# Kernel tuning notes

Hardware: AMD Instinct MI355X
Metric: run time of the kernel (lower is better)

## Reference

```python
import jax, jax.numpy as jnp
import numpy as np

HEADS = 12
DIM_HEAD = 64
SCALE = DIM_HEAD ** -0.5


def _attn(q, k, v):
    # q: [B, I, D], k/v: [B, J, D]
    sim = jnp.einsum('bid,bjd->bij', q, k)
    a = jax.nn.softmax(sim, axis=-1)
    out = jnp.einsum('bij,bjd->bid', a, v)
    return out, a


def setup_inputs() -> dict:
    key = jax.random.key(0)
    k1, k2, k3 = jax.random.split(key, 3)
    B, F, N, DIM = 8, 8, 196, 768
    x = jax.random.normal(k1, (B, 1 + F * N, DIM), dtype=jnp.float32)
    W_qkv = jax.random.normal(k2, (DIM, 3 * HEADS * DIM_HEAD), dtype=jnp.float32) * (DIM ** -0.5)
    W_out = jax.random.normal(k3, (HEADS * DIM_HEAD, DIM), dtype=jnp.float32) * ((HEADS * DIM_HEAD) ** -0.5)
    b_out = jnp.zeros((DIM,), dtype=jnp.float32)
    return {"x": x, "W_qkv": W_qkv, "W_out": W_out, "b_out": b_out, "f": F}


def reference(x, W_qkv, W_out, b_out, f):
    b, n_tot, dim = x.shape
    h, d = HEADS, DIM_HEAD
    qkv = x @ W_qkv                              # [b, n, 3*h*d]
    q, k, v = jnp.split(qkv, 3, axis=-1)
    # 'b n (h d) -> (b h) n d'
    def to_bh(t):
        return t.reshape(b, n_tot, h, d).transpose(0, 2, 1, 3).reshape(b * h, n_tot, d)
    q, k, v = map(to_bh, (q, k, v))
    q = q * SCALE
    cls_q, q_ = q[:, :1], q[:, 1:]
    cls_k, k_ = k[:, :1], k[:, 1:]
    cls_v, v_ = v[:, :1], v[:, 1:]
    # cls token attends over full sequence
    cls_out, cls_attn = _attn(cls_q, k, v)       # [(b h), 1, d], [(b h), 1, n_tot]
    # spatial attention: 'b (f n) d -> (b f) n d'
    bh = b * h
    n = (n_tot - 1) // f
    def to_bf(t):
        return t.reshape(bh, f, n, d).reshape(bh * f, n, d)
    q_, k_, v_ = map(to_bf, (q_, k_, v_))
    r = f  # q_.shape[0] // cls_k.shape[0]
    # repeat 'b () d -> (b r) () d'
    cls_k_r = jnp.repeat(cls_k, r, axis=0)       # [(bh f), 1, d]
    cls_v_r = jnp.repeat(cls_v, r, axis=0)
    k_ = jnp.concatenate((cls_k_r, k_), axis=1)  # [(bh f), 1+n, d]
    v_ = jnp.concatenate((cls_v_r, v_), axis=1)
    out, _ = _attn(q_, k_, v_)                   # [(bh f), n, d]
    # '(b f) n d -> b (f n) d' (with b := bh)
    out = out.reshape(bh, f * n, d)
    out = jnp.concatenate((cls_out, out), axis=1)  # [(b h), n_tot, d]
    # '(b h) n d -> b n (h d)'
    out = out.reshape(b, h, n_tot, d).transpose(0, 2, 1, 3).reshape(b, n_tot, h * d)
    return out @ W_out + b_out, cls_attn
```

## Files before the change

kernel.cpp:

```cpp
#include <hip/hip_runtime.h>

typedef unsigned short u16;
typedef unsigned int u32;
typedef __attribute__((ext_vector_type(8))) short s16x8;
typedef __attribute__((ext_vector_type(4))) float f32x4;
typedef __attribute__((ext_vector_type(4))) u32 u32x4;
typedef __attribute__((ext_vector_type(4))) float fvec4;

#define DEV static __device__ __forceinline__

typedef __attribute__((address_space(1))) unsigned char ga_u8;
typedef __attribute__((address_space(3))) unsigned char la_u8;

DEV u16 f2bf(float f){
  u32 u = __builtin_bit_cast(u32, f);
  u32 r = (u + 0x7FFFu + ((u >> 16) & 1u)) >> 16;
  return (u16)r;
}
DEV float bf2f(u16 v){
  u32 x = ((u32)v) << 16;
  return __builtin_bit_cast(float, x);
}
DEV f32x4 mfma16(s16x8 a, s16x8 b, f32x4 c){
  return __builtin_amdgcn_mfma_f32_16x16x32_bf16(a, b, c, 0, 0, 0);
}
DEV s16x8 ld16B(const u16* p){
  return __builtin_bit_cast(s16x8, *(const u32x4*)p);
}
DEV u32 cvt_pk_bf16(float lo, float hi){
  u32 r;
  asm volatile("v_cvt_pk_bf16_f32 %0, %1, %2" : "=v"(r) : "v"(lo), "v"(hi));
  return r;
}
DEV void gload16(const void* g, void* l){
  __builtin_amdgcn_global_load_lds((const ga_u8*)g, (la_u8*)l, 16, 0, 0);
}
DEV int xcd_chunk(int bid, int nwg){
  int q = nwg >> 3, r = nwg & 7;
  int xcd = bid & 7, lin = bid >> 3;
  return (xcd < r ? xcd*(q+1) : r*(q+1) + (xcd-r)*q) + lin;
}

#define BARRIER() __builtin_amdgcn_s_barrier()
#define LGKM0()   asm volatile("s_waitcnt lgkmcnt(0)" ::: "memory")
#define VMC4()    asm volatile("s_waitcnt vmcnt(4)" ::: "memory")
#define VMC0()    asm volatile("s_waitcnt vmcnt(0)" ::: "memory")


__global__ __launch_bounds__(256) void k_cvt(const float* __restrict__ in, u16* __restrict__ out, int n4){
  int i = blockIdx.x*256 + threadIdx.x;
  int stride = gridDim.x*256;
  for (; i < n4; i += stride){
    fvec4 v = ((const fvec4*)in)[i];
    u16 o0 = f2bf(v[0]), o1 = f2bf(v[1]), o2 = f2bf(v[2]), o3 = f2bf(v[3]);
    u32 lo = (u32)o0 | ((u32)o1 << 16);
    u32 hi = (u32)o2 | ((u32)o3 << 16);
    ((u32*)out)[2*i]   = lo;
    ((u32*)out)[2*i+1] = hi;
  }
}

__global__ __launch_bounds__(256) void k_transpose(const float* __restrict__ W, u16* __restrict__ WT, int K, int N){
  __shared__ float tile[32][33];
  int bn = blockIdx.x * 32;
  int bk = blockIdx.y * 32;
  int tx = threadIdx.x & 31, ty = threadIdx.x >> 5;
  #pragma unroll
  for (int r = ty; r < 32; r += 8)
    tile[r][tx] = W[(size_t)(bk + r)*N + bn + tx];
  __syncthreads();
  #pragma unroll
  for (int r = ty; r < 32; r += 8)
    WT[(size_t)(bn + r)*K + bk + tx] = f2bf(tile[tx][r]);
}

__global__ __launch_bounds__(512, 2) void gemm_qkv(const u16* __restrict__ A, const u16* __restrict__ BT,
                                                   u16* __restrict__ qout, u16* __restrict__ kout, u16* __restrict__ vout){
  __shared__ u16 sA[2][2][128*64];
  __shared__ u16 sB[2][2][128*64];
  const int M = 12552;
  const int NWG = 50*9;
  int logical = xcd_chunk(blockIdx.x, NWG);
  int bxi = logical % 9, byi = logical / 9;
  int bm = byi * 256, bn = bxi * 256;

  int tid = threadIdx.x;
  int w = tid >> 6, l = tid & 63, l15 = l & 15, l4 = l >> 4;
  int wm = w >> 2, wn = w & 3;
  int swz = (l15 & 7) << 3;

  f32x4 acc[8][4];
  #pragma unroll
  for (int a=0;a<8;a++)
    #pragma unroll
    for (int b=0;b<4;b++) acc[a][b] = (f32x4){0.f,0.f,0.f,0.f};

  auto stageA = [&](int dbuf, int h, int kt){
    #pragma unroll
    for (int i=0;i<2;i++){
      int ci = i*512 + tid;
      int cs = ci ^ ((ci>>3)&7);
      int r = cs>>3, cc = (cs&7)*8;
      int gr = bm + h*128 + r; if (gr >= M) gr = M-1;
      gload16(A + (size_t)gr*768 + kt*64 + cc, &sA[dbuf][h][(i*512 + (w<<6))*8]);
    }
  };
  auto stageB = [&](int dbuf, int h, int kt){
    #pragma unroll
    for (int i=0;i<2;i++){
      int ci = i*512 + tid;
      int cs = ci ^ ((ci>>3)&7);
      int r = cs>>3, cc = (cs&7)*8;
      gload16(BT + (size_t)(bn + h*128 + r)*768 + kt*64 + cc, &sB[dbuf][h][(i*512 + (w<<6))*8]);
    }
  };

  s16x8 af[4][2], bf[4][2];
  #define LDA_(d, mi, kk) ld16B(&sA[d][wm][(((mi)*16 + l15)*64 + (kk)*32 + l4*8) ^ swz])
  #define LDB_(d, ni, kk) ld16B(&sB[d][(wn*64 + (ni)*16 + l15)>>7][((((wn*64 + (ni)*16 + l15)&127))*64 + (kk)*32 + l4*8) ^ swz])
  #define QUAD(MH, NH) do{ \
    __builtin_amdgcn_s_setprio(1); \
    _Pragma("unroll") \
    for (int j=0;j<4;j++){ \
      _Pragma("unroll") \
      for (int n=0;n<2;n++){ \
        acc[(MH)*4+j][(NH)*2+n] = mfma16(af[j][0], bf[(NH)*2+n][0], acc[(MH)*4+j][(NH)*2+n]); \
        acc[(MH)*4+j][(NH)*2+n] = mfma16(af[j][1], bf[(NH)*2+n][1], acc[(MH)*4+j][(NH)*2+n]); \
      } } \
    __builtin_amdgcn_s_setprio(0); }while(0)

  stageA(0,0,0); stageA(0,1,0); stageB(0,0,0); stageB(0,1,0);
  stageA(1,0,1); stageA(1,1,1);
  VMC4();
  BARRIER();

  #pragma unroll 1
  for (int it = 0; it < 6; ++it){
    int kt1 = 2*it + 1;
    bool full = (it < 5);
    #pragma unroll
    for (int j=0;j<4;j++){ af[j][0]=LDA_(0,j,0); af[j][1]=LDA_(0,j,1); }
    #pragma unroll
    for (int n=0;n<2;n++){ bf[n][0]=LDB_(0,n,0); bf[n][1]=LDB_(0,n,1); }
    stageB(1, 0, kt1);
    BARRIER(); LGKM0();
    QUAD(0,0);
    BARRIER();
    #pragma unroll
    for (int n=2;n<4;n++){ bf[n][0]=LDB_(0,n,0); bf[n][1]=LDB_(0,n,1); }
    stageB(1, 1, kt1);
    BARRIER(); LGKM0();
    QUAD(0,1);
    BARRIER();
    #pragma unroll
    for (int j=0;j<4;j++){ af[j][0]=LDA_(0,4+j,0); af[j][1]=LDA_(0,4+j,1); }
    if (full) stageA(0, 0, kt1+1);
    BARRIER(); LGKM0();
    QUAD(1,0);
    BARRIER();
    if (full) stageA(0, 1, kt1+1);
    BARRIER();
    QUAD(1,1);
    if (full) { VMC4(); } else { VMC0(); }
    BARRIER();
    #pragma unroll
    for (int j=0;j<4;j++){ af[j][0]=LDA_(1,j,0); af[j][1]=LDA_(1,j,1); }
    #pragma unroll
    for (int n=0;n<2;n++){ bf[n][0]=LDB_(1,n,0); bf[n][1]=LDB_(1,n,1); }
    if (full) stageB(0, 0, kt1+1);
    BARRIER(); LGKM0();
    QUAD(0,0);
    BARRIER();
    #pragma unroll
    for (int n=2;n<4;n++){ bf[n][0]=LDB_(1,n,0); bf[n][1]=LDB_(1,n,1); }
    if (full) stageB(0, 1, kt1+1);
    BARRIER(); LGKM0();
    QUAD(0,1);
    BARRIER();
    #pragma unroll
    for (int j=0;j<4;j++){ af[j][0]=LDA_(1,4+j,0); af[j][1]=LDA_(1,4+j,1); }
    if (full) stageA(1, 0, kt1+2);
    BARRIER(); LGKM0();
    QUAD(1,0);
    BARRIER();
    if (full) stageA(1, 1, kt1+2);
    BARRIER();
    QUAD(1,1);
    if (full) VMC4();
    BARRIER();
  }
  #undef LDA_
  #undef LDB_
  #undef QUAD

  int which = bn / 768;
  int h = ((bn - which*768) >> 6) + wn;
  u16* dst  = (which==0) ? qout : ((which==1) ? kout : vout);
  float scale = (which==0) ? 0.125f : 1.f;
  #pragma unroll
  for (int mi=0; mi<8; mi++){
    #pragma unroll
    for (int r=0; r<4; r++){
      int m = bm + wm*128 + mi*16 + l4*4 + r;
      if (m >= M) continue;
      int b = m / 1569, t = m - b*1569;
      u16* drow = dst + ((size_t)(b*12 + h)*1569 + t)*64 + l15;
      #pragma unroll
      for (int n=0; n<4; n++)
        drow[n*16] = f2bf(acc[mi][n][r] * scale);
    }
  }
}

__global__ __launch_bounds__(256) void cls_sim(const u16* __restrict__ qb, const u16* __restrict__ kb,
                                               float* __restrict__ sim, float* __restrict__ bmax){
  int c = blockIdx.x, g = blockIdx.y;
  int tid = threadIdx.x;
  __shared__ float qv[64];
  __shared__ float red[256];
  if (tid < 64) qv[tid] = bf2f(qb[(size_t)g*1569*64 + tid]);
  __syncthreads();
  int j = c*256 + tid;
  float s = -1e30f;
  if (j < 1569){
    const u16* kr = kb + ((size_t)g*1569 + j)*64;
    float a = 0.f;
    #pragma unroll
    for (int d0 = 0; d0 < 64; d0 += 8){
      u32x4 u = *(const u32x4*)(kr + d0);
      const u16* us = (const u16*)&u;
      #pragma unroll
      for (int i=0;i<8;i++) a += qv[d0+i]*bf2f(us[i]);
    }
    s = a;
    sim[(size_t)g*1569 + j] = s;
  }
  red[tid] = s; __syncthreads();
  for (int st=128; st>0; st>>=1){ if (tid<st) red[tid] = fmaxf(red[tid], red[tid+st]); __syncthreads(); }
  if (tid == 0) bmax[g*8 + c] = red[0];
}

__global__ __launch_bounds__(256) void cls_fin(float* __restrict__ sim, const float* __restrict__ bmax,
                                               float* __restrict__ attn){
  int g = blockIdx.x, tid = threadIdx.x;
  __shared__ float red[256];
  float m = -1e30f;
  #pragma unroll
  for (int c=0;c<7;c++) m = fmaxf(m, bmax[g*8+c]);
  float ls = 0.f;
  for (int j = tid; j < 1569; j += 256){
    float e = expf(sim[(size_t)g*1569+j] - m);
    sim[(size_t)g*1569+j] = e;
    ls += e;
  }
  red[tid] = ls; __syncthreads();
  for (int st=128; st>0; st>>=1){ if (tid<st) red[tid] += red[tid+st]; __syncthreads(); }
  float inv = 1.f/red[0];
  for (int j = tid; j < 1569; j += 256)
    attn[(size_t)g*1569+j] = sim[(size_t)g*1569+j]*inv;
}

__global__ __launch_bounds__(256) void cls_pv(const float* __restrict__ attn, const u16* __restrict__ vb,
                                              float* __restrict__ pvp){
  int c = blockIdx.x, g = blockIdx.y;
  int tid = threadIdx.x;
  int d = tid & 63, kk = tid >> 6;
  __shared__ float red[256];
  float a = 0.f;
  for (int jj = kk; jj < 256; jj += 4){
    int j = c*256 + jj;
    if (j < 1569) a += attn[(size_t)g*1569+j] * bf2f(vb[((size_t)g*1569+j)*64 + d]);
  }
  red[tid] = a; __syncthreads();
  if (tid < 64) pvp[((size_t)g*7 + c)*64 + tid] = red[tid]+red[tid+64]+red[tid+128]+red[tid+192];
}

__global__ __launch_bounds__(64) void cls_pv_red(const float* __restrict__ pvp, u16* __restrict__ ob){
  int g = blockIdx.x, d = threadIdx.x;
  float s = 0.f;
  #pragma unroll
  for (int c=0;c<7;c++) s += pvp[((size_t)g*7+c)*64 + d];
  ob[(size_t)g*1569*64 + d] = f2bf(s);
}

__global__ __launch_bounds__(256) void k_frame(const u16* __restrict__ qb, const u16* __restrict__ kb,
                                               const u16* __restrict__ vb, u16* __restrict__ ob){
  int g = blockIdx.x;
  int bh = g >> 3, fi = g & 7;
  int tid = threadIdx.x;
  int w = tid >> 6, l = tid & 63;
  int l15 = l & 15, l4 = l >> 4;

  __shared__ u16 Ks[208][72];
  __shared__ u16 Vt[64][232];
  __shared__ u16 Ps[4][64][40];

  const u16* qg = qb + ((size_t)bh*1569 + 1 + fi*196)*64;
  const u16* kg = kb + (size_t)bh*1569*64;
  const u16* vg = vb + (size_t)bh*1569*64;

  {
    int jj = tid >> 3, c = (tid & 7)*8;
    #pragma unroll
    for (int base = 0; base < 224; base += 32){
      int j = base + jj;
      u32x4 kv = {0,0,0,0}, vv = {0,0,0,0};
      if (j < 197){
        int t = (j == 0) ? 0 : (1 + fi*196 + j - 1);
        kv = *(const u32x4*)(kg + (size_t)t*64 + c);
        vv = *(const u32x4*)(vg + (size_t)t*64 + c);
      }
      if (j < 208) *(u32x4*)&Ks[j][c] = kv;
      int jl = j & 31;
      int col = (j & ~31) + ((jl & 15)*2 + (jl >> 4));
      const u16* vp = (const u16*)&vv;
      #pragma unroll
      for (int i=0;i<8;i++) Vt[c+i][col] = vp[i];
    }
  }

  s16x8 qf[4][2];
  #pragma unroll
  for (int mt=0; mt<4; mt++){
    int row = w*64 + mt*16 + l15;
    #pragma unroll
    for (int kk=0; kk<2; kk++){
      if (row < 196) qf[mt][kk] = ld16B(qg + (size_t)row*64 + kk*32 + l4*8);
      else { u32x4 z = {0,0,0,0}; qf[mt][kk] = __builtin_bit_cast(s16x8, z); }
    }
  }

  f32x4 acc[4][4];
  float rsum[4][4];
  #pragma unroll
  for (int a=0;a<4;a++)
    #pragma unroll
    for (int b=0;b<4;b++){ acc[a][b] = (f32x4){0.f,0.f,0.f,0.f}; rsum[a][b] = 0.f; }

  __syncthreads();

  for (int ck = 0; ck < 7; ck++){
    int r0 = ck*32 + l15;
    int r1 = r0 + 16; if (r1 > 207) r1 = 207;
    s16x8 kf0[2], kf1[2];
    #pragma unroll
    for (int kk=0; kk<2; kk++){
      kf0[kk] = ld16B(&Ks[r0][kk*32 + l4*8]);
      kf1[kk] = ld16B(&Ks[r1][kk*32 + l4*8]);
    }
    bool ok0 = (ck*32 + l15) < 197;
    bool ok1 = (ck*32 + 16 + l15) < 197;

    #pragma unroll
    for (int mt=0; mt<4; mt++){
      __builtin_amdgcn_s_setprio(1);
      f32x4 s0 = (f32x4){0.f,0.f,0.f,0.f}, s1 = (f32x4){0.f,0.f,0.f,0.f};
      s0 = mfma16(qf[mt][0], kf0[0], s0);
      s0 = mfma16(qf[mt][1], kf0[1], s0);
      s1 = mfma16(qf[mt][0], kf1[0], s1);
      s1 = mfma16(qf[mt][1], kf1[1], s1);
      __builtin_amdgcn_s_setprio(0);
      #pragma unroll
      for (int r=0; r<4; r++){
        float p0 = ok0 ? __expf(s0[r] - 8.f) : 0.f;
        float p1 = ok1 ? __expf(s1[r] - 8.f) : 0.f;
        rsum[mt][r] += p0 + p1;
        int prow = mt*16 + l4*4 + r;
        *(u32*)&Ps[w][prow][2*l15] = cvt_pk_bf16(p0, p1);
      }
    }

    s16x8 vf[4];
    #pragma unroll
    for (int ntd=0; ntd<4; ntd++) vf[ntd] = ld16B(&Vt[ntd*16 + l15][ck*32 + l4*8]);
    #pragma unroll
    for (int mt=0; mt<4; mt++){
      s16x8 pf = ld16B(&Ps[w][mt*16 + l15][l4*8]);
      __builtin_amdgcn_s_setprio(1);
      #pragma unroll
      for (int ntd=0; ntd<4; ntd++)
        acc[mt][ntd] = mfma16(pf, vf[ntd], acc[mt][ntd]);
      __builtin_amdgcn_s_setprio(0);
    }
  }

  u16* og = ob + ((size_t)bh*1569 + 1 + fi*196)*64;
  #pragma unroll
  for (int mt=0; mt<4; mt++){
    #pragma unroll
    for (int r=0; r<4; r++){
      float rs = rsum[mt][r];
      rs += __shfl_xor(rs, 1);
      rs += __shfl_xor(rs, 2);
      rs += __shfl_xor(rs, 4);
      rs += __shfl_xor(rs, 8);
      int row = w*64 + mt*16 + l4*4 + r;
      if (row < 196){
        float inv = 1.f / rs;
        #pragma unroll
        for (int ntd=0; ntd<4; ntd++)
          og[(size_t)row*64 + ntd*16 + l15] = f2bf(acc[mt][ntd][r] * inv);
      }
    }
  }
}

__global__ __launch_bounds__(512, 2) void gemm_out(const u16* __restrict__ AO, const u16* __restrict__ BT,
                                                   const float* __restrict__ bias, float* __restrict__ C){
  __shared__ u16 sA[2][2][128*64];
  __shared__ u16 sB[2][2][128*64];
  const int M = 12552;
  const int NWG = 50*3;
  int logical = xcd_chunk(blockIdx.x, NWG);
  int bxi = logical % 3, byi = logical / 3;
  int bm = byi * 256, bn = bxi * 256;

  int tid = threadIdx.x;
  int w = tid >> 6, l = tid & 63, l15 = l & 15, l4 = l >> 4;
  int wm = w >> 2, wn = w & 3;
  int swz = (l15 & 7) << 3;

  f32x4 acc[8][4];
  #pragma unroll
  for (int a=0;a<8;a++)
    #pragma unroll
    for (int b=0;b<4;b++) acc[a][b] = (f32x4){0.f,0.f,0.f,0.f};

  auto stageA = [&](int dbuf, int h, int kt){
    #pragma unroll
    for (int i=0;i<2;i++){
      int ci = i*512 + tid;
      int cs = ci ^ ((ci>>3)&7);
      int r = cs>>3, cc = (cs&7)*8;
      int gr = bm + h*128 + r; if (gr >= M) gr = M-1;
      int b = gr / 1569, t = gr - b*1569;
      gload16(AO + ((size_t)(b*12 + kt)*1569 + t)*64 + cc, &sA[dbuf][h][(i*512 + (w<<6))*8]);
    }
  };
  auto stageB = [&](int dbuf, int h, int kt){
    #pragma unroll
    for (int i=0;i<2;i++){
      int ci = i*512 + tid;
      int cs = ci ^ ((ci>>3)&7);
      int r = cs>>3, cc = (cs&7)*8;
      gload16(BT + (size_t)(bn + h*128 + r)*768 + kt*64 + cc, &sB[dbuf][h][(i*512 + (w<<6))*8]);
    }
  };

  s16x8 af[4][2], bf[4][2];
  #define LDA_(d, mi, kk) ld16B(&sA[d][wm][(((mi)*16 + l15)*64 + (kk)*32 + l4*8) ^ swz])
  #define LDB_(d, ni, kk) ld16B(&sB[d][(wn*64 + (ni)*16 + l15)>>7][((((wn*64 + (ni)*16 + l15)&127))*64 + (kk)*32 + l4*8) ^ swz])
  #define QUAD(MH, NH) do{ \
    __builtin_amdgcn_s_setprio(1); \
    _Pragma("unroll") \
    for (int j=0;j<4;j++){ \
      _Pragma("unroll") \
      for (int n=0;n<2;n++){ \
        acc[(MH)*4+j][(NH)*2+n] = mfma16(af[j][0], bf[(NH)*2+n][0], acc[(MH)*4+j][(NH)*2+n]); \
        acc[(MH)*4+j][(NH)*2+n] = mfma16(af[j][1], bf[(NH)*2+n][1], acc[(MH)*4+j][(NH)*2+n]); \
      } } \
    __builtin_amdgcn_s_setprio(0); }while(0)

  stageA(0,0,0); stageA(0,1,0); stageB(0,0,0); stageB(0,1,0);
  stageA(1,0,1); stageA(1,1,1);
  VMC4();
  BARRIER();

  #pragma unroll 1
  for (int it = 0; it < 6; ++it){
    int kt1 = 2*it + 1;
    bool full = (it < 5);
    #pragma unroll
    for (int j=0;j<4;j++){ af[j][0]=LDA_(0,j,0); af[j][1]=LDA_(0,j,1); }
    #pragma unroll
    for (int n=0;n<2;n++){ bf[n][0]=LDB_(0,n,0); bf[n][1]=LDB_(0,n,1); }
    stageB(1, 0, kt1);
    BARRIER(); LGKM0();
    QUAD(0,0);
    BARRIER();
    #pragma unroll
    for (int n=2;n<4;n++){ bf[n][0]=LDB_(0,n,0); bf[n][1]=LDB_(0,n,1); }
    stageB(1, 1, kt1);
    BARRIER(); LGKM0();
    QUAD(0,1);
    BARRIER();
    #pragma unroll
    for (int j=0;j<4;j++){ af[j][0]=LDA_(0,4+j,0); af[j][1]=LDA_(0,4+j,1); }
    if (full) stageA(0, 0, kt1+1);
    BARRIER(); LGKM0();
    QUAD(1,0);
    BARRIER();
    if (full) stageA(0, 1, kt1+1);
    BARRIER();
    QUAD(1,1);
    if (full) { VMC4(); } else { VMC0(); }
    BARRIER();
    #pragma unroll
    for (int j=0;j<4;j++){ af[j][0]=LDA_(1,j,0); af[j][1]=LDA_(1,j,1); }
    #pragma unroll
    for (int n=0;n<2;n++){ bf[n][0]=LDB_(1,n,0); bf[n][1]=LDB_(1,n,1); }
    if (full) stageB(0, 0, kt1+1);
    BARRIER(); LGKM0();
    QUAD(0,0);
    BARRIER();
    #pragma unroll
    for (int n=2;n<4;n++){ bf[n][0]=LDB_(1,n,0); bf[n][1]=LDB_(1,n,1); }
    if (full) stageB(0, 1, kt1+1);
    BARRIER(); LGKM0();
    QUAD(0,1);
    BARRIER();
    #pragma unroll
    for (int j=0;j<4;j++){ af[j][0]=LDA_(1,4+j,0); af[j][1]=LDA_(1,4+j,1); }
    if (full) stageA(1, 0, kt1+2);
    BARRIER(); LGKM0();
    QUAD(1,0);
    BARRIER();
    if (full) stageA(1, 1, kt1+2);
    BARRIER();
    QUAD(1,1);
    if (full) VMC4();
    BARRIER();
  }
  #undef LDA_
  #undef LDB_
  #undef QUAD

  int n0 = bn + wn*64;
  float bv[4];
  #pragma unroll
  for (int n=0;n<4;n++) bv[n] = bias[n0 + n*16 + l15];
  #pragma unroll
  for (int mi=0; mi<8; mi++){
    #pragma unroll
    for (int r=0; r<4; r++){
      int m = bm + wm*128 + mi*16 + l4*4 + r;
      if (m >= M) continue;
      float* crow = C + (size_t)m*768 + n0 + l15;
      #pragma unroll
      for (int n=0; n<4; n++)
        crow[n*16] = acc[mi][n][r] + bv[n];
    }
  }
}

extern "C" void kernel_launch(void* const* d_in, const int* in_sizes, int n_in,
                              void* d_out, int out_size, void* d_ws, size_t ws_size,
                              hipStream_t stream){
  (void)in_sizes; (void)n_in; (void)out_size;
  const float* x    = (const float*)d_in[0];
  const float* Wqkv = (const float*)d_in[1];
  const float* Wout = (const float*)d_in[2];
  const float* bout = (const float*)d_in[3];
  float* out0 = (float*)d_out;
  float* out1 = out0 + (size_t)12552*768;

  char* ws = (char*)d_ws;
  size_t off = 0;
  auto alloc = [&](size_t bytes)->char*{
    char* p = ws + off;
    off += (bytes + 255) & ~(size_t)255;
    return p;
  };
  u16* xb    = (u16*)alloc((size_t)12552*768*2);
  u16* wqkvT = (u16*)alloc((size_t)2304*768*2);
  u16* woutT = (u16*)alloc((size_t)768*768*2);
  u16* qb    = (u16*)alloc((size_t)96*1569*64*2);
  u16* kbuf  = (u16*)alloc((size_t)96*1569*64*2);
  u16* vbuf  = (u16*)alloc((size_t)96*1569*64*2);
  u16* ao    = (u16*)alloc((size_t)96*1569*64*2);
  float* simw = (float*)alloc((size_t)96*1569*4);
  float* bmax = (float*)alloc((size_t)96*8*4);
  float* pvp  = (float*)alloc((size_t)96*7*64*4);
  if (off > ws_size) return;

  k_cvt<<<2048, 256, 0, stream>>>(x, xb, 12552*768/4);
  k_transpose<<<dim3(72, 24), 256, 0, stream>>>(Wqkv, wqkvT, 768, 2304);
  k_transpose<<<dim3(24, 24), 256, 0, stream>>>(Wout, woutT, 768, 768);
  gemm_qkv<<<50*9, 512, 0, stream>>>(xb, wqkvT, qb, kbuf, vbuf);
  cls_sim<<<dim3(7, 96), 256, 0, stream>>>(qb, kbuf, simw, bmax);
  cls_fin<<<96, 256, 0, stream>>>(simw, bmax, out1);
  cls_pv<<<dim3(7, 96), 256, 0, stream>>>(out1, vbuf, pvp);
  cls_pv_red<<<96, 64, 0, stream>>>(pvp, ao);
  k_frame<<<768, 256, 0, stream>>>(qb, kbuf, vbuf, ao);
  gemm_out<<<50*3, 512, 0, stream>>>(ao, woutT, bout, out0);
}
```

Measured before the change: 183.5 us.

## Fuse prep kernels, merge CLS softmax and PV, keep P in registers

The three input-prep kernels (x conversion and two weight transposes) become one launch. The CLS softmax normalisation, PV product and reduction become a single per-group kernel that keeps the exponentials in LDS. In the frame attention kernel the QK MFMA operands are swapped so the P tile comes out already in the register layout the PV MFMA needs, and Vt is permuted to match. This removes the P round trip through LDS and changes the row-sum reduction to use LDS. The costs are fewer launches and less LDS traffic, but the fused CLS tail runs only 96 blocks serially over 1569 keys, which may lose parallelism.

```diff
diff --git a/kernel.cpp b/kernel.cpp
--- a/kernel.cpp
+++ b/kernel.cpp
@@ -47,24 +47,31 @@
 #define VMC0()    asm volatile("s_waitcnt vmcnt(0)" ::: "memory")
 
 
-__global__ __launch_bounds__(256) void k_cvt(const float* __restrict__ in, u16* __restrict__ out, int n4){
-  int i = blockIdx.x*256 + threadIdx.x;
-  int stride = gridDim.x*256;
-  for (; i < n4; i += stride){
-    fvec4 v = ((const fvec4*)in)[i];
-    u16 o0 = f2bf(v[0]), o1 = f2bf(v[1]), o2 = f2bf(v[2]), o3 = f2bf(v[3]);
-    u32 lo = (u32)o0 | ((u32)o1 << 16);
-    u32 hi = (u32)o2 | ((u32)o3 << 16);
-    ((u32*)out)[2*i]   = lo;
-    ((u32*)out)[2*i+1] = hi;
-  }
-}
-
-__global__ __launch_bounds__(256) void k_transpose(const float* __restrict__ W, u16* __restrict__ WT, int K, int N){
+__global__ __launch_bounds__(256) void k_prep(const float* __restrict__ x, u16* __restrict__ xb,
+                                              const float* __restrict__ Wqkv, u16* __restrict__ wqkvT,
+                                              const float* __restrict__ Wout, u16* __restrict__ woutT){
   __shared__ float tile[32][33];
-  int bn = blockIdx.x * 32;
-  int bk = blockIdx.y * 32;
-  int tx = threadIdx.x & 31, ty = threadIdx.x >> 5;
+  int b = blockIdx.x, tid = threadIdx.x;
+  if (b < 2048){
+    const int n4 = 12552*768/4;
+    for (int i = b*256 + tid; i < n4; i += 2048*256){
+      fvec4 v = ((const fvec4*)x)[i];
+      u32 lo = (u32)f2bf(v[0]) | ((u32)f2bf(v[1]) << 16);
+      u32 hi = (u32)f2bf(v[2]) | ((u32)f2bf(v[3]) << 16);
+      ((u32*)xb)[2*i]   = lo;
+      ((u32*)xb)[2*i+1] = hi;
+    }
+    return;
+  }
+  const float* W; u16* WT; int K, N, bn, bk;
+  if (b < 2048 + 1728){
+    int bb = b - 2048; W = Wqkv; WT = wqkvT; K = 768; N = 2304;
+    bn = (bb % 72) * 32; bk = (bb / 72) * 32;
+  } else {
+    int bb = b - 3776; W = Wout; WT = woutT; K = 768; N = 768;
+    bn = (bb % 24) * 32; bk = (bb / 24) * 32;
+  }
+  int tx = tid & 31, ty = tid >> 5;
   #pragma unroll
   for (int r = ty; r < 32; r += 8)
     tile[r][tx] = W[(size_t)(bk + r)*N + bn + tx];
@@ -240,47 +247,34 @@
   if (tid == 0) bmax[g*8 + c] = red[0];
 }
 
-__global__ __launch_bounds__(256) void cls_fin(float* __restrict__ sim, const float* __restrict__ bmax,
-                                               float* __restrict__ attn){
+__global__ __launch_bounds__(256) void cls_tail(const float* __restrict__ sim, const float* __restrict__ bmax,
+                                                const u16* __restrict__ vb, float* __restrict__ attn,
+                                                u16* __restrict__ ob){
   int g = blockIdx.x, tid = threadIdx.x;
+  __shared__ float e_lds[1569];
   __shared__ float red[256];
   float m = -1e30f;
   #pragma unroll
   for (int c=0;c<7;c++) m = fmaxf(m, bmax[g*8+c]);
   float ls = 0.f;
   for (int j = tid; j < 1569; j += 256){
-    float e = expf(sim[(size_t)g*1569+j] - m);
-    sim[(size_t)g*1569+j] = e;
+    float e = __expf(sim[(size_t)g*1569+j] - m);
+    e_lds[j] = e;
     ls += e;
   }
   red[tid] = ls; __syncthreads();
   for (int st=128; st>0; st>>=1){ if (tid<st) red[tid] += red[tid+st]; __syncthreads(); }
   float inv = 1.f/red[0];
   for (int j = tid; j < 1569; j += 256)
-    attn[(size_t)g*1569+j] = sim[(size_t)g*1569+j]*inv;
-}
-
-__global__ __launch_bounds__(256) void cls_pv(const float* __restrict__ attn, const u16* __restrict__ vb,
-                                              float* __restrict__ pvp){
-  int c = blockIdx.x, g = blockIdx.y;
-  int tid = threadIdx.x;
-  int d = tid & 63, kk = tid >> 6;
-  __shared__ float red[256];
+    attn[(size_t)g*1569+j] = e_lds[j]*inv;
+  __syncthreads();
+  int d = tid & 63, part = tid >> 6;
   float a = 0.f;
-  for (int jj = kk; jj < 256; jj += 4){
-    int j = c*256 + jj;
-    if (j < 1569) a += attn[(size_t)g*1569+j] * bf2f(vb[((size_t)g*1569+j)*64 + d]);
-  }
+  for (int j = part; j < 1569; j += 4)
+    a += e_lds[j] * bf2f(vb[((size_t)g*1569+j)*64 + d]);
   red[tid] = a; __syncthreads();
-  if (tid < 64) pvp[((size_t)g*7 + c)*64 + tid] = red[tid]+red[tid+64]+red[tid+128]+red[tid+192];
-}
-
-__global__ __launch_bounds__(64) void cls_pv_red(const float* __restrict__ pvp, u16* __restrict__ ob){
-  int g = blockIdx.x, d = threadIdx.x;
-  float s = 0.f;
-  #pragma unroll
-  for (int c=0;c<7;c++) s += pvp[((size_t)g*7+c)*64 + d];
-  ob[(size_t)g*1569*64 + d] = f2bf(s);
+  if (tid < 64)
+    ob[(size_t)g*1569*64 + tid] = f2bf((red[tid]+red[tid+64]+red[tid+128]+red[tid+192]) * inv);
 }
 
 __global__ __launch_bounds__(256) void k_frame(const u16* __restrict__ qb, const u16* __restrict__ kb,
@@ -293,7 +287,7 @@
 
   __shared__ u16 Ks[208][72];
   __shared__ u16 Vt[64][232];
-  __shared__ u16 Ps[4][64][40];
+  __shared__ float rs_lds[4][64];
 
   const u16* qg = qb + ((size_t)bh*1569 + 1 + fi*196)*64;
   const u16* kg = kb + (size_t)bh*1569*64;
@@ -312,7 +306,7 @@
       }
       if (j < 208) *(u32x4*)&Ks[j][c] = kv;
       int jl = j & 31;
-      int col = (j & ~31) + ((jl & 15)*2 + (jl >> 4));
+      int col = (j & ~31) + ((jl>>2)&3)*8 + (jl>>4)*4 + (jl&3);
       const u16* vp = (const u16*)&vv;
       #pragma unroll
       for (int i=0;i<8;i++) Vt[c+i][col] = vp[i];
@@ -331,11 +325,11 @@
   }
 
   f32x4 acc[4][4];
-  float rsum[4][4];
+  float rsum[4] = {0.f, 0.f, 0.f, 0.f};
   #pragma unroll
   for (int a=0;a<4;a++)
     #pragma unroll
-    for (int b=0;b<4;b++){ acc[a][b] = (f32x4){0.f,0.f,0.f,0.f}; rsum[a][b] = 0.f; }
+    for (int b=0;b<4;b++) acc[a][b] = (f32x4){0.f,0.f,0.f,0.f};
 
   __syncthreads();
 
@@ -348,55 +342,57 @@
       kf0[kk] = ld16B(&Ks[r0][kk*32 + l4*8]);
       kf1[kk] = ld16B(&Ks[r1][kk*32 + l4*8]);
     }
-    bool ok0 = (ck*32 + l15) < 197;
-    bool ok1 = (ck*32 + 16 + l15) < 197;
+    s16x8 vf[4];
+    #pragma unroll
+    for (int ntd=0; ntd<4; ntd++) vf[ntd] = ld16B(&Vt[ntd*16 + l15][ck*32 + l4*8]);
+    int kbase = ck*32 + l4*4;
 
     #pragma unroll
     for (int mt=0; mt<4; mt++){
       __builtin_amdgcn_s_setprio(1);
       f32x4 s0 = (f32x4){0.f,0.f,0.f,0.f}, s1 = (f32x4){0.f,0.f,0.f,0.f};
-      s0 = mfma16(qf[mt][0], kf0[0], s0);
-      s0 = mfma16(qf[mt][1], kf0[1], s0);
-      s1 = mfma16(qf[mt][0], kf1[0], s1);
-      s1 = mfma16(qf[mt][1], kf1[1], s1);
+      s0 = mfma16(kf0[0], qf[mt][0], s0);
+      s0 = mfma16(kf0[1], qf[mt][1], s0);
+      s1 = mfma16(kf1[0], qf[mt][0], s1);
+      s1 = mfma16(kf1[1], qf[mt][1], s1);
       __builtin_amdgcn_s_setprio(0);
+      float p[8];
       #pragma unroll
       for (int r=0; r<4; r++){
-        float p0 = ok0 ? __expf(s0[r] - 8.f) : 0.f;
-        float p1 = ok1 ? __expf(s1[r] - 8.f) : 0.f;
-        rsum[mt][r] += p0 + p1;
-        int prow = mt*16 + l4*4 + r;
-        *(u32*)&Ps[w][prow][2*l15] = cvt_pk_bf16(p0, p1);
+        p[r]   = (kbase + r      < 197) ? __expf(s0[r] - 8.f) : 0.f;
+        p[4+r] = (kbase + 16 + r < 197) ? __expf(s1[r] - 8.f) : 0.f;
       }
-    }
-
-    s16x8 vf[4];
-    #pragma unroll
-    for (int ntd=0; ntd<4; ntd++) vf[ntd] = ld16B(&Vt[ntd*16 + l15][ck*32 + l4*8]);
-    #pragma unroll
-    for (int mt=0; mt<4; mt++){
-      s16x8 pf = ld16B(&Ps[w][mt*16 + l15][l4*8]);
+      rsum[mt] += ((p[0]+p[1])+(p[2]+p[3])) + ((p[4]+p[5])+(p[6]+p[7]));
+      u32x4 pw;
+      pw[0] = cvt_pk_bf16(p[0], p[1]);
+      pw[1] = cvt_pk_bf16(p[2], p[3]);
+      pw[2] = cvt_pk_bf16(p[4], p[5]);
+      pw[3] = cvt_pk_bf16(p[6], p[7]);
+      s16x8 pa = __builtin_bit_cast(s16x8, pw);
       __builtin_amdgcn_s_setprio(1);
       #pragma unroll
       for (int ntd=0; ntd<4; ntd++)
-        acc[mt][ntd] = mfma16(pf, vf[ntd], acc[mt][ntd]);
+        acc[mt][ntd] = mfma16(pa, vf[ntd], acc[mt][ntd]);
       __builtin_amdgcn_s_setprio(0);
     }
   }
 
+  #pragma unroll
+  for (int mt=0; mt<4; mt++){
+    float rs = rsum[mt];
+    rs += __shfl_xor(rs, 16);
+    rs += __shfl_xor(rs, 32);
+    rs_lds[w][mt*16 + l15] = rs;
+  }
+
   u16* og = ob + ((size_t)bh*1569 + 1 + fi*196)*64;
   #pragma unroll
   for (int mt=0; mt<4; mt++){
     #pragma unroll
     for (int r=0; r<4; r++){
-      float rs = rsum[mt][r];
-      rs += __shfl_xor(rs, 1);
-      rs += __shfl_xor(rs, 2);
-      rs += __shfl_xor(rs, 4);
-      rs += __shfl_xor(rs, 8);
       int row = w*64 + mt*16 + l4*4 + r;
       if (row < 196){
-        float inv = 1.f / rs;
+        float inv = 1.f / rs_lds[w][mt*16 + l4*4 + r];
         #pragma unroll
         for (int ntd=0; ntd<4; ntd++)
           og[(size_t)row*64 + ntd*16 + l15] = f2bf(acc[mt][ntd][r] * inv);
@@ -570,17 +566,12 @@
   u16* ao    = (u16*)alloc((size_t)96*1569*64*2);
   float* simw = (float*)alloc((size_t)96*1569*4);
   float* bmax = (float*)alloc((size_t)96*8*4);
-  float* pvp  = (float*)alloc((size_t)96*7*64*4);
   if (off > ws_size) return;
 
-  k_cvt<<<2048, 256, 0, stream>>>(x, xb, 12552*768/4);
-  k_transpose<<<dim3(72, 24), 256, 0, stream>>>(Wqkv, wqkvT, 768, 2304);
-  k_transpose<<<dim3(24, 24), 256, 0, stream>>>(Wout, woutT, 768, 768);
+  k_prep<<<4352, 256, 0, stream>>>(x, xb, Wqkv, wqkvT, Wout, woutT);
   gemm_qkv<<<50*9, 512, 0, stream>>>(xb, wqkvT, qb, kbuf, vbuf);
   cls_sim<<<dim3(7, 96), 256, 0, stream>>>(qb, kbuf, simw, bmax);
-  cls_fin<<<96, 256, 0, stream>>>(simw, bmax, out1);
-  cls_pv<<<dim3(7, 96), 256, 0, stream>>>(out1, vbuf, pvp);
-  cls_pv_red<<<96, 64, 0, stream>>>(pvp, ao);
+  cls_tail<<<96, 256, 0, stream>>>(simw, bmax, vbuf, out1, ao);
   k_frame<<<768, 256, 0, stream>>>(qb, kbuf, vbuf, ao);
   gemm_out<<<50*3, 512, 0, stream>>>(ao, woutT, bout, out0);
 }
```

Result: slower. 244.1 us (+33.0%).
